# Performance work log

Hardware: AMD Instinct MI355X
Metric: run time of the kernel (lower is better)

## Reference

```python
import jax, jax.numpy as jnp
import numpy as np

B, S, DIM, HEADS, HD, FF = 2, 2048, 1024, 16, 64, 4096
PREV, MAX_SEQ, THETA, POS_BIAS_MAX, EPS = 1024, 4096, 10000.0, 2.0, 1e-6


def _freqs_cos_sin():
    inv = 1.0 / THETA ** (np.arange(0, HD, 2)[: HD // 2].astype(np.float32) / HD)
    f = np.outer(np.arange(MAX_SEQ, dtype=np.float32), inv)
    return jnp.asarray(np.cos(f), jnp.float32), jnp.asarray(np.sin(f), jnp.float32)


def setup_inputs():
    key = jax.random.key(0)
    ks = jax.random.split(key, 16)
    lin = lambda k, o, i: 0.02 * jax.random.normal(k, (o, i), jnp.float32)
    cos, sin = _freqs_cos_sin()
    return {
        "x": jax.random.normal(ks[0], (B, S, DIM), jnp.float32),
        "cache_k": jax.random.normal(ks[1], (B, HEADS, PREV, HD), jnp.float32),
        "cache_v": jax.random.normal(ks[2], (B, HEADS, PREV, HD), jnp.float32),
        "cos": cos, "sin": sin,
        "attn_norm_w": jnp.ones((DIM,), jnp.float32),
        "ffn_norm_w": jnp.ones((DIM,), jnp.float32),
        "wq": lin(ks[3], DIM, DIM), "bq": jnp.zeros((DIM,), jnp.float32),
        "wk": lin(ks[4], DIM, DIM), "bk": jnp.zeros((DIM,), jnp.float32),
        "wv": lin(ks[5], DIM, DIM), "bv": jnp.zeros((DIM,), jnp.float32),
        "wo": lin(ks[6], DIM, DIM), "bo": jnp.zeros((DIM,), jnp.float32),
        "w_gate": lin(ks[7], FF, DIM), "b_gate": jnp.zeros((FF,), jnp.float32),
        "w_value": lin(ks[8], FF, DIM), "b_value": jnp.zeros((FF,), jnp.float32),
        "w_proj": lin(ks[9], DIM, FF), "b_proj": jnp.zeros((DIM,), jnp.float32),
        "cache_limit": 3072,
    }


def _rmsnorm(h, w):
    return h * jax.lax.rsqrt(jnp.mean(h * h, axis=-1, keepdims=True) + EPS) * w


def _rope(t, cos, sin):
    # t: [B,H,L,HD]; cos/sin: [L, HD//2]; rotate interleaved pairs (complex mult)
    t2 = t.reshape(t.shape[:-1] + (HD // 2, 2))
    x0, x1 = t2[..., 0], t2[..., 1]
    c = cos[None, None]
    s = sin[None, None]
    out = jnp.stack([x0 * c - x1 * s, x0 * s + x1 * c], axis=-1)
    return out.reshape(t.shape)


def _forward(x, cache_k, cache_v, cos, sin, attn_norm_w, ffn_norm_w, wq, bq, wk, bk, wv, bv, wo, bo, w_gate, b_gate, w_value, b_value, w_proj, b_proj, cache_limit):
    b, s, d = x.shape
    h = _rmsnorm(x, attn_norm_w)
    shape4 = lambda t: t.reshape(b, s, HEADS, HD).transpose(0, 2, 1, 3)  # [B,H,S,HD]
    q = shape4(h @ wq.T + bq)
    k_new = shape4(h @ wk.T + bk)
    v_new = shape4(h @ wv.T + bv)
    k_all = jnp.concatenate([cache_k, k_new], axis=2)
    v_all = jnp.concatenate([cache_v, v_new], axis=2)
    if cache_limit > 0:
        k_all = k_all[:, :, -cache_limit:, :]
        v_all = v_all[:, :, -cache_limit:, :]
    total = k_all.shape[2]
    prev = total - s
    # RoPE: q at absolute positions prev..prev+s-1, keys at 0..total-1 (mod cache len)
    pos_q = (jnp.arange(s) + prev) % MAX_SEQ
    pos_k = jnp.arange(total) % MAX_SEQ
    q = _rope(q, cos[pos_q], sin[pos_q])
    k = _rope(k_all, cos[pos_k], sin[pos_k])
    # linear positional bias + causal mask over the new-token block only
    slope = POS_BIAS_MAX / max(total - 1, 1)
    j = jnp.arange(total, dtype=jnp.float32)[None, :]
    i_abs = (prev + jnp.arange(s, dtype=jnp.float32))[:, None]
    bias = slope * (j - i_abs)  # [s, total]
    causal = (jnp.arange(total)[None, :] - prev) > jnp.arange(s)[:, None]
    mask = jnp.where(causal, -jnp.inf, bias)
    scores = jnp.einsum('bhsd,bhtd->bhst', q, k) / jnp.sqrt(jnp.float32(HD)) + mask
    attn = jax.nn.softmax(scores, axis=-1)
    ctx = jnp.einsum('bhst,bhtd->bhsd', attn, v_all)
    ctx = ctx.transpose(0, 2, 1, 3).reshape(b, s, d)
    x = x + ctx @ wo.T + bo
    h2 = _rmsnorm(x, ffn_norm_w)
    gated = jax.nn.silu(h2 @ w_gate.T + b_gate) * (h2 @ w_value.T + b_value)
    return x + gated @ w_proj.T + b_proj


def reference(x, cache_k, cache_v, cos, sin, attn_norm_w, ffn_norm_w, wq, bq, wk, bk, wv, bv, wo, bo, w_gate, b_gate, w_value, b_value, w_proj, b_proj, cache_limit):
    return _forward(x, cache_k, cache_v, cos, sin, attn_norm_w, ffn_norm_w, wq, bq, wk, bk, wv, bv, wo, bo, w_gate, b_gate, w_value, b_value, w_proj, b_proj, cache_limit)
```

## Files before the change

kernel.cpp:

```cpp
#include <hip/hip_runtime.h>
#include <stdint.h>

typedef unsigned short u16;
typedef unsigned int   u32;
typedef __bf16 bf16x8 __attribute__((ext_vector_type(8)));
typedef float  f32x4  __attribute__((ext_vector_type(4)));
typedef u32    u32x4  __attribute__((ext_vector_type(4)));
typedef u32    u32x2  __attribute__((ext_vector_type(2)));

#define B_SZ  2
#define S_LEN 2048
#define NH    16
#define HD    64
#define DIM   1024
#define FF    4096
#define T_LEN 3072
#define PREV  1024
#define MROWS (B_SZ * S_LEN)
#define LOG2E 1.44269504f

#define MFMA16 __builtin_amdgcn_mfma_f32_16x16x32_bf16

__device__ __forceinline__ u16 f2bf(float f) {
  u32 u = __builtin_bit_cast(u32, f);
  u32 r = u + 0x7FFFu + ((u >> 16) & 1u);
  return (u16)(r >> 16);
}
__device__ __forceinline__ float bf2f(u16 h) {
  u32 u = ((u32)h) << 16;
  return __builtin_bit_cast(float, u);
}
__device__ __forceinline__ u32 cvtpk(float lo, float hi) {
  u32 r;
  asm("v_cvt_pk_bf16_f32 %0, %1, %2" : "=v"(r) : "v"(lo), "v"(hi));
  return r;
}

__device__ __forceinline__ void gl_lds16(const void* g, void* l) {
  __builtin_amdgcn_global_load_lds(
      (const __attribute__((address_space(1))) u32*)g,
      (__attribute__((address_space(3))) u32*)l, 16, 0, 0);
}

#define GFENCE() asm volatile("" ::: "memory")
#define BARF()                         \
  do {                                 \
    GFENCE();                          \
    __builtin_amdgcn_s_barrier();      \
    GFENCE();                          \
  } while (0)

__global__ __launch_bounds__(256) void cvt_kernel(const float* __restrict__ src,
                                                  u16* __restrict__ dst, int n4) {
  int i = blockIdx.x * 256 + threadIdx.x;
  const int stride = gridDim.x * 256;
  for (; i < n4; i += stride) {
    f32x4 v = *(const f32x4*)&src[(long)i * 4];
    u32x2 o;
    o[0] = (u32)f2bf(v[0]) | ((u32)f2bf(v[1]) << 16);
    o[1] = (u32)f2bf(v[2]) | ((u32)f2bf(v[3]) << 16);
    *(u32x2*)&dst[(long)i * 4] = o;
  }
}

__global__ __launch_bounds__(256) void cvt_sw_kernel(const float* __restrict__ src,
                                                     u16* __restrict__ dst, int nunits) {
  int i = blockIdx.x * 256 + threadIdx.x;
  const int stride = gridDim.x * 256;
  for (; i < nunits; i += stride) {
    int row = i >> 7;
    int g = i & 127;
    const float* s = &src[((long)row << 10) + g * 8];
    f32x4 a = *(const f32x4*)s;
    f32x4 b = *(const f32x4*)(s + 4);
    u32x4 o;
    o[0] = (u32)f2bf(a[0]) | ((u32)f2bf(a[1]) << 16);
    o[1] = (u32)f2bf(a[2]) | ((u32)f2bf(a[3]) << 16);
    o[2] = (u32)f2bf(b[0]) | ((u32)f2bf(b[1]) << 16);
    o[3] = (u32)f2bf(b[2]) | ((u32)f2bf(b[3]) << 16);
    const int gp = (g & ~7) | ((g & 7) ^ (row & 7));
    *(u32x4*)&dst[((long)row << 10) + gp * 8] = o;
  }
}

__global__ __launch_bounds__(256) void cvt_ilv_sw_kernel(const float* __restrict__ wg,
                                                         const float* __restrict__ wval,
                                                         u16* __restrict__ dst) {
  int i = blockIdx.x * 256 + threadIdx.x;
  const int stride = gridDim.x * 256;
  for (; i < FF * 128; i += stride) {
    int j = i >> 7;
    int g = i & 127;
    const float* sg = &wg[((long)j << 10) + g * 8];
    const float* sv = &wval[((long)j << 10) + g * 8];
    f32x4 a = *(const f32x4*)sg;
    f32x4 b = *(const f32x4*)(sg + 4);
    u32x4 og;
    og[0] = (u32)f2bf(a[0]) | ((u32)f2bf(a[1]) << 16);
    og[1] = (u32)f2bf(a[2]) | ((u32)f2bf(a[3]) << 16);
    og[2] = (u32)f2bf(b[0]) | ((u32)f2bf(b[1]) << 16);
    og[3] = (u32)f2bf(b[2]) | ((u32)f2bf(b[3]) << 16);
    f32x4 c = *(const f32x4*)sv;
    f32x4 d = *(const f32x4*)(sv + 4);
    u32x4 ov;
    ov[0] = (u32)f2bf(c[0]) | ((u32)f2bf(c[1]) << 16);
    ov[1] = (u32)f2bf(c[2]) | ((u32)f2bf(c[3]) << 16);
    ov[2] = (u32)f2bf(d[0]) | ((u32)f2bf(d[1]) << 16);
    ov[3] = (u32)f2bf(d[2]) | ((u32)f2bf(d[3]) << 16);
    const int rg = 2 * j, rv = 2 * j + 1;
    const int gpg = (g & ~7) | ((g & 7) ^ (rg & 7));
    const int gpv = (g & ~7) | ((g & 7) ^ (rv & 7));
    *(u32x4*)&dst[((long)rg << 10) + gpg * 8] = og;
    *(u32x4*)&dst[((long)rv << 10) + gpv * 8] = ov;
  }
}

__global__ __launch_bounds__(256) void bias_ilv_kernel(const float* __restrict__ bg,
                                                       const float* __restrict__ bval,
                                                       float* __restrict__ dst) {
  int i = blockIdx.x * 256 + threadIdx.x;
  if (i < FF) {
    dst[2 * i] = bg[i];
    dst[2 * i + 1] = bval[i];
  }
}

__global__ __launch_bounds__(256) void rmsnorm_kernel(const float* __restrict__ x,
                                                      const float* __restrict__ w,
                                                      u16* __restrict__ out) {
  const int row = blockIdx.x;
  const int tid = threadIdx.x;
  const long base = (long)row * DIM + tid * 4;
  f32x4 v = *(const f32x4*)&x[base];
  float ss = v[0] * v[0] + v[1] * v[1] + v[2] * v[2] + v[3] * v[3];
#pragma unroll
  for (int d = 1; d <= 32; d <<= 1) ss += __shfl_xor(ss, d, 64);
  __shared__ float red[4];
  if ((tid & 63) == 0) red[tid >> 6] = ss;
  __syncthreads();
  float tot = red[0] + red[1] + red[2] + red[3];
  const float sc = rsqrtf(tot * (1.f / (float)DIM) + 1e-6f);
  f32x4 wv4 = *(const f32x4*)&w[tid * 4];
  u32x2 o;
  o[0] = (u32)f2bf(v[0] * sc * wv4[0]) | ((u32)f2bf(v[1] * sc * wv4[1]) << 16);
  o[1] = (u32)f2bf(v[2] * sc * wv4[2]) | ((u32)f2bf(v[3] * sc * wv4[3]) << 16);
  const int u = tid >> 1, hf = tid & 1;
  const int up = (u & 0x78) | ((u & 7) ^ (row & 7));
  *(u32x2*)&out[(long)row * DIM + up * 8 + hf * 4] = o;
}

template <int EPI>
__global__ __launch_bounds__(512, 2) void gemm256(const u16* __restrict__ A,
                                                  const u16* __restrict__ Bw,
                                                  const float* __restrict__ bias,
                                                  u16* __restrict__ out_bf,
                                                  int N, int K) {
  __shared__ __align__(16) u16 Ab[2][256 * 64];
  __shared__ __align__(16) u16 Bb[2][256 * 64];
  const int tid = threadIdx.x;
  const int lane = tid & 63;
  const int wid = tid >> 6;
  const int wm = wid >> 2, wn = wid & 3;
  const int l15 = lane & 15, lhi = lane >> 4;
  const int c7 = l15 & 7;
  const long m0 = (long)blockIdx.y * 256;
  const long n0 = (long)blockIdx.x * 256;
  const int NT = K >> 6;

  const int srow = tid >> 3;
  const int sunit = (tid & 7) * 8;
  const u16* agp = A + (m0 + srow) * K + sunit;
  const u16* bgp = Bw + (n0 + srow) * K + sunit;
  const int ldst = tid * 8;

  auto stageA = [&](int kt, int b) {
    const int k0 = kt << 6;
    u16* d = &Ab[b][0];
#pragma unroll
    for (int c = 0; c < 4; ++c)
      gl_lds16(agp + (long)(c * 64) * K + k0, d + c * 4096 + ldst);
  };
  auto stageB = [&](int kt, int b) {
    const int k0 = kt << 6;
    u16* d = &Bb[b][0];
#pragma unroll
    for (int c = 0; c < 4; ++c)
      gl_lds16(bgp + (long)(c * 64) * K + k0, d + c * 4096 + ldst);
  };

#define READ_A(MH)                                                               \
  _Pragma("unroll") for (int m_ = 0; m_ < 4; ++m_) {                             \
    _Pragma("unroll") for (int ks_ = 0; ks_ < 2; ++ks_) {                        \
      Afr[MH][m_ * 2 + ks_] =                                                    \
          *(const bf16x8*)&Ac[(wm * 128 + (MH)*64 + m_ * 16 + l15) * 64 +        \
                              (((ks_ * 4 + lhi) ^ c7) * 8)];                     \
    }                                                                            \
  }
#define READ_B(NH)                                                               \
  _Pragma("unroll") for (int n_ = 0; n_ < 2; ++n_) {                             \
    _Pragma("unroll") for (int ks_ = 0; ks_ < 2; ++ks_) {                        \
      Bfr[NH][n_ * 2 + ks_] =                                                    \
          *(const bf16x8*)&Bc[(wn * 64 + (NH)*32 + n_ * 16 + l15) * 64 +         \
                              (((ks_ * 4 + lhi) ^ c7) * 8)];                     \
    }                                                                            \
  }
#define QUAD(MH, NH)                                                             \
  do {                                                                           \
    __builtin_amdgcn_s_setprio(1);                                               \
    _Pragma("unroll") for (int m_ = 0; m_ < 4; ++m_) {                           \
      _Pragma("unroll") for (int n_ = 0; n_ < 2; ++n_) {                         \
        acc[(MH)*4 + m_][(NH)*2 + n_] =                                          \
            MFMA16(Afr[MH][m_ * 2], Bfr[NH][n_ * 2],                             \
                   acc[(MH)*4 + m_][(NH)*2 + n_], 0, 0, 0);                      \
        acc[(MH)*4 + m_][(NH)*2 + n_] =                                          \
            MFMA16(Afr[MH][m_ * 2 + 1], Bfr[NH][n_ * 2 + 1],                     \
                   acc[(MH)*4 + m_][(NH)*2 + n_], 0, 0, 0);                      \
      }                                                                          \
    }                                                                            \
    __builtin_amdgcn_s_setprio(0);                                               \
  } while (0)

  f32x4 acc[8][4] = {};

  stageA(0, 0);
  stageB(0, 0);
  stageA(1, 1);
  stageB(1, 1);
  asm volatile("s_waitcnt vmcnt(8)" ::: "memory");
  __builtin_amdgcn_s_barrier();
  GFENCE();

  for (int kt = 0; kt < NT; ++kt) {
    const int b = kt & 1;
    const u16* Ac = &Ab[b][0];
    const u16* Bc = &Bb[b][0];
    bf16x8 Afr[2][8], Bfr[2][4];
    READ_A(0);
    READ_B(0);
    BARF();
    QUAD(0, 0);
    BARF();
    READ_A(1);
    READ_B(1);
    BARF();
    QUAD(0, 1);
    BARF();
    if (kt + 2 < NT) stageA(kt + 2, b);
    BARF();
    QUAD(1, 0);
    BARF();
    if (kt + 2 < NT) stageB(kt + 2, b);
    BARF();
    QUAD(1, 1);
    if (kt + 1 < NT) {
      if (kt + 2 < NT)
        asm volatile("s_waitcnt vmcnt(8)" ::: "memory");
      else
        asm volatile("s_waitcnt vmcnt(0)" ::: "memory");
      __builtin_amdgcn_s_barrier();
      GFENCE();
    }
  }
#undef READ_A
#undef READ_B
#undef QUAD

#pragma unroll
  for (int mi = 0; mi < 8; ++mi) {
    const long row0 = m0 + wm * 128 + mi * 16 + lhi * 4;
#pragma unroll
    for (int ni = 0; ni < 4; ++ni) {
      const long col = n0 + wn * 64 + ni * 16 + l15;
      const float bb = bias[col];
#pragma unroll
      for (int r = 0; r < 4; ++r) {
        float v = acc[mi][ni][r] + bb;
        if (EPI == 2) {
          float other = __shfl_xor(v, 1, 64);
          if (!(l15 & 1)) {
            float s = v / (1.f + __expf(-v)) * other;
            out_bf[(row0 + r) * (N >> 1) + (col >> 1)] = f2bf(s);
          }
        } else {
          out_bf[(row0 + r) * N + col] = f2bf(v);
        }
      }
    }
  }
}

template <int EPI, int NB>
__global__ __launch_bounds__(256) void gemm_bt(const u16* __restrict__ A,
                                               const u16* __restrict__ Bw,
                                               const float* __restrict__ bias,
                                               const float* __restrict__ resid,
                                               u16* __restrict__ out_bf,
                                               float* __restrict__ out_f,
                                               int N, int K) {
  constexpr int BHALF = NB / 64;
  constexpr int NFR = NB / 32;
  constexpr int LPT = 2 + BHALF;
  __shared__ __align__(16) u16 As[3][128 * 32];
  __shared__ __align__(16) u16 Bs[3][NB * 32];
  const int tid = threadIdx.x;
  const int lane = tid & 63;
  const int wv = tid >> 6;
  const int wr = wv >> 1, wc = wv & 1;
  const long m0 = (long)blockIdx.y * 128;
  const long n0 = (long)blockIdx.x * NB;

  const int arow = tid >> 2;
  const int acol = (tid & 3) << 3;
  const u16* ag = A + (m0 + arow) * K + acol;
  const u16* bg = Bw + (n0 + arow) * K + acol;
  const long hK = (long)64 * K;

  f32x4 acc[4][NFR] = {};
  const int l15 = lane & 15;
  const int lhi = lane >> 4;
  const int aoff0 = (wr * 64 + l15) * 32 + lhi * 8;
  const int boff0 = (wc * (NB / 2) + l15) * 32 + lhi * 8;
  const int nk = K >> 5;

  auto stage = [&](int t, int buf) {
    const int k0 = t << 5;
    gl_lds16(ag + k0, &As[buf][tid * 8]);
    gl_lds16(ag + k0 + hK, &As[buf][2048 + tid * 8]);
    gl_lds16(bg + k0, &Bs[buf][tid * 8]);
    if (BHALF == 2) gl_lds16(bg + k0 + hK, &Bs[buf][2048 + tid * 8]);
  };

  stage(0, 0);
  stage(1, 1);
  asm volatile("s_waitcnt vmcnt(%0)" ::"n"(LPT) : "memory");
  __builtin_amdgcn_s_barrier();
  GFENCE();

  for (int t = 0; t < nk; ++t) {
    const int cb = t % 3;
    if (t + 2 < nk) stage(t + 2, (t + 2) % 3);
    bf16x8 af[4], bfr[NFR];
#pragma unroll
    for (int i = 0; i < 4; ++i) af[i] = *(const bf16x8*)&As[cb][aoff0 + i * 16 * 32];
#pragma unroll
    for (int j = 0; j < NFR; ++j) bfr[j] = *(const bf16x8*)&Bs[cb][boff0 + j * 16 * 32];
    __builtin_amdgcn_s_setprio(1);
#pragma unroll
    for (int i = 0; i < 4; ++i)
#pragma unroll
      for (int j = 0; j < NFR; ++j)
        acc[i][j] = MFMA16(af[i], bfr[j], acc[i][j], 0, 0, 0);
    __builtin_amdgcn_s_setprio(0);
    if (t + 2 < nk) {
      asm volatile("s_waitcnt vmcnt(%0)" ::"n"(LPT) : "memory");
      __builtin_amdgcn_s_barrier();
      GFENCE();
    } else if (t + 1 < nk) {
      asm volatile("s_waitcnt vmcnt(0)" ::: "memory");
      __builtin_amdgcn_s_barrier();
      GFENCE();
    }
  }

#pragma unroll
  for (int i = 0; i < 4; ++i) {
    const long row0 = m0 + wr * 64 + i * 16 + lhi * 4;
#pragma unroll
    for (int j = 0; j < NFR; ++j) {
      const long col = n0 + wc * (NB / 2) + j * 16 + l15;
      const float bb = bias[col];
#pragma unroll
      for (int r = 0; r < 4; ++r) {
        const long idx = (row0 + r) * N + col;
        float v = acc[i][j][r] + bb;
        if (EPI == 0) out_bf[idx] = f2bf(v);
        else          out_f[idx] = resid[idx] + v;
      }
    }
  }
}

__global__ __launch_bounds__(256) void rope_q_kernel(const u16* __restrict__ qkv,
                                                     const float* __restrict__ cosT,
                                                     const float* __restrict__ sinT,
                                                     u16* __restrict__ Q) {
  int idx = blockIdx.x * 256 + threadIdx.x;
  int u = idx & 7;
  int s = (idx >> 3) & (S_LEN - 1);
  int bh = idx >> 14;
  int b = bh >> 4, h = bh & 15;
  int pos = PREV + s;
  const float SC = 0.125f * LOG2E;
  const u16* src = qkv + ((long)(b * S_LEN + s)) * (3 * DIM) + h * HD + u * 8;
  u32x4 d = *(const u32x4*)src;
  f32x4 cv = *(const f32x4*)&cosT[(long)pos * 32 + u * 4];
  f32x4 sv = *(const f32x4*)&sinT[(long)pos * 32 + u * 4];
  u32x4 o;
#pragma unroll
  for (int p = 0; p < 4; ++p) {
    float x0 = bf2f((u16)(d[p] & 0xffff));
    float x1 = bf2f((u16)(d[p] >> 16));
    float y0 = (x0 * cv[p] - x1 * sv[p]) * SC;
    float y1 = (x0 * sv[p] + x1 * cv[p]) * SC;
    o[p] = (u32)f2bf(y0) | ((u32)f2bf(y1) << 16);
  }
  *(u32x4*)&Q[((long)bh * S_LEN + s) * HD + u * 8] = o;
}

__global__ __launch_bounds__(256) void rope_k_kernel(const u16* __restrict__ qkv,
                                                     const float* __restrict__ cache_k,
                                                     const float* __restrict__ cosT,
                                                     const float* __restrict__ sinT,
                                                     u16* __restrict__ Kall) {
  int idx = blockIdx.x * 256 + threadIdx.x;
  int u = idx & 7;
  int t2 = idx >> 3;
  int j = t2 % T_LEN;
  int bh = t2 / T_LEN;
  int b = bh >> 4, h = bh & 15;
  float e[8];
  if (j < PREV) {
    const float* src = cache_k + ((long)bh * PREV + j) * HD + u * 8;
    f32x4 a = *(const f32x4*)src;
    f32x4 c = *(const f32x4*)(src + 4);
    e[0] = a[0]; e[1] = a[1]; e[2] = a[2]; e[3] = a[3];
    e[4] = c[0]; e[5] = c[1]; e[6] = c[2]; e[7] = c[3];
  } else {
    const u16* src = qkv + ((long)(b * S_LEN + (j - PREV))) * (3 * DIM) + DIM + h * HD + u * 8;
    u32x4 d = *(const u32x4*)src;
#pragma unroll
    for (int p = 0; p < 4; ++p) {
      e[2 * p] = bf2f((u16)(d[p] & 0xffff));
      e[2 * p + 1] = bf2f((u16)(d[p] >> 16));
    }
  }
  f32x4 cv = *(const f32x4*)&cosT[(long)j * 32 + u * 4];
  f32x4 sv = *(const f32x4*)&sinT[(long)j * 32 + u * 4];
  u32x4 o;
#pragma unroll
  for (int p = 0; p < 4; ++p) {
    float y0 = e[2 * p] * cv[p] - e[2 * p + 1] * sv[p];
    float y1 = e[2 * p] * sv[p] + e[2 * p + 1] * cv[p];
    o[p] = (u32)f2bf(y0) | ((u32)f2bf(y1) << 16);
  }
  *(u32x4*)&Kall[((long)bh * T_LEN + j) * HD + (u ^ (j & 7)) * 8] = o;
}

__global__ __launch_bounds__(256) void build_vt_kernel(const u16* __restrict__ qkv,
                                                       const float* __restrict__ cache_v,
                                                       u16* __restrict__ Vtg) {
  int idx = blockIdx.x * 256 + threadIdx.x;
  int hd = idx & 63;
  int t2 = idx >> 6;
  int kb = t2 % 384;
  int bh = t2 / 384;
  int b = bh >> 4, h = bh & 15;
  int key0 = kb * 8;
  u16 vals[8];
  if (key0 < PREV) {
#pragma unroll
    for (int i = 0; i < 8; ++i)
      vals[i] = f2bf(cache_v[((long)bh * PREV + key0 + i) * HD + hd]);
  } else {
#pragma unroll
    for (int i = 0; i < 8; ++i)
      vals[i] = qkv[((long)(b * S_LEN + key0 + i - PREV)) * (3 * DIM) + 2 * DIM + h * HD + hd];
  }
  u32x4 o;
#pragma unroll
  for (int p = 0; p < 4; ++p)
    o[p] = (u32)vals[2 * p] | ((u32)vals[2 * p + 1] << 16);
  const int span = kb >> 3;
  const int u = (kb & 7) ^ (hd & 7);
  *(u32x4*)&Vtg[((long)bh * HD + hd) * T_LEN + span * 64 + u * 8] = o;
}

__global__ __launch_bounds__(256, 4) void attn_kernel(const u16* __restrict__ Q,
                                                      const u16* __restrict__ Kg,
                                                      const u16* __restrict__ Vtg,
                                                      u16* __restrict__ ctx, float slope2) {
  __shared__ __align__(16) u16 Ks[2][64 * 64];
  __shared__ __align__(16) u16 Vs[2][64 * 64];
  __shared__ __align__(16) u16 Ps[4][16 * 64];

  const int tid = threadIdx.x;
  const int lane = tid & 63;
  const int wv = tid >> 6;
  const int l15 = lane & 15;
  const int lhi = lane >> 4;
  const int c7 = l15 & 7;
  const int bh = blockIdx.x;
  const int qt = blockIdx.y;
  const int b = bh >> 4, h = bh & 15;
  const int q0 = qt * 64;
  const int nt = (PREV + q0 + 64) >> 6;

  const long qrow = (long)bh * S_LEN + q0 + wv * 16 + l15;
  bf16x8 aq0 = *(const bf16x8*)&Q[qrow * HD + lhi * 8];
  bf16x8 aq1 = *(const bf16x8*)&Q[qrow * HD + 32 + lhi * 8];

  const long kgb = (long)bh * T_LEN * HD;
  const long vgb = (long)bh * HD * T_LEN;
  const int srow = tid >> 3;
  const int sunit = (tid & 7) * 8;

  gl_lds16(&Kg[kgb + (long)srow * HD + sunit], &Ks[0][tid * 8]);
  gl_lds16(&Kg[kgb + (long)(srow + 32) * HD + sunit], &Ks[0][2048 + tid * 8]);
  gl_lds16(&Vtg[vgb + (long)srow * T_LEN + sunit], &Vs[0][tid * 8]);
  gl_lds16(&Vtg[vgb + (long)(srow + 32) * T_LEN + sunit], &Vs[0][2048 + tid * 8]);
  __syncthreads();

  f32x4 o[4] = {};
  float mrun = -1e30f, lrun = 0.f;
  const int iabs = PREV + q0 + wv * 16 + l15;
  u16* Pw = &Ps[wv][0];

  for (int t = 0; t < nt; ++t) {
    const int cur = t & 1, nxt = cur ^ 1;
    const int kt0 = t << 6;
    if (t + 1 < nt) {
      const int kn = kt0 + 64;
      gl_lds16(&Kg[kgb + (long)(kn + srow) * HD + sunit], &Ks[nxt][tid * 8]);
      gl_lds16(&Kg[kgb + (long)(kn + srow + 32) * HD + sunit], &Ks[nxt][2048 + tid * 8]);
      gl_lds16(&Vtg[vgb + (long)srow * T_LEN + kn + sunit], &Vs[nxt][tid * 8]);
      gl_lds16(&Vtg[vgb + (long)(srow + 32) * T_LEN + kn + sunit], &Vs[nxt][2048 + tid * 8]);
    }

    f32x4 sf[4];
    __builtin_amdgcn_s_setprio(1);
#pragma unroll
    for (int jf = 0; jf < 4; ++jf) {
      const int krow = jf * 16 + l15;
      bf16x8 ak0 = *(const bf16x8*)&Ks[cur][krow * 64 + ((lhi ^ c7) * 8)];
      bf16x8 ak1 = *(const bf16x8*)&Ks[cur][krow * 64 + (((4 + lhi) ^ c7) * 8)];
      f32x4 s = {};
      s = MFMA16(ak0, aq0, s, 0, 0, 0);
      s = MFMA16(ak1, aq1, s, 0, 0, 0);
      sf[jf] = s;
    }
    __builtin_amdgcn_s_setprio(0);

    const bool masked = (t == nt - 1);
#pragma unroll
    for (int jf = 0; jf < 4; ++jf)
#pragma unroll
      for (int r = 0; r < 4; ++r) {
        const int jcol = kt0 + jf * 16 + 4 * lhi + r;
        float s_ = sf[jf][r] + slope2 * (float)(jcol - iabs);
        sf[jf][r] = (masked && jcol > iabs) ? -1e30f : s_;
      }

    float t0 = fmaxf(fmaxf(sf[0][0], sf[0][1]), fmaxf(sf[0][2], sf[0][3]));
    float t1 = fmaxf(fmaxf(sf[1][0], sf[1][1]), fmaxf(sf[1][2], sf[1][3]));
    float t2 = fmaxf(fmaxf(sf[2][0], sf[2][1]), fmaxf(sf[2][2], sf[2][3]));
    float t3 = fmaxf(fmaxf(sf[3][0], sf[3][1]), fmaxf(sf[3][2], sf[3][3]));
    float pmax = fmaxf(fmaxf(t0, t1), fmaxf(t2, t3));
    pmax = fmaxf(pmax, __shfl_xor(pmax, 16, 64));
    pmax = fmaxf(pmax, __shfl_xor(pmax, 32, 64));

    if (!__all(pmax - mrun <= 8.f)) {
      float mnew = fmaxf(mrun, pmax);
      float scl = exp2f(mrun - mnew);
      mrun = mnew;
      lrun *= scl;
#pragma unroll
      for (int r = 0; r < 4; ++r) {
        float sr = __shfl(scl, 4 * lhi + r, 64);
#pragma unroll
        for (int hf = 0; hf < 4; ++hf) o[hf][r] *= sr;
      }
    }

    float ps = 0.f;
#pragma unroll
    for (int jf = 0; jf < 4; ++jf) {
      f32x4 p;
#pragma unroll
      for (int r = 0; r < 4; ++r) {
        p[r] = exp2f(sf[jf][r] - mrun);
        ps += p[r];
      }
      u32x2 pw2;
      pw2[0] = cvtpk(p[0], p[1]);
      pw2[1] = cvtpk(p[2], p[3]);
      const int u = (2 * jf + (lhi >> 1)) ^ c7;
      *(u32x2*)&Pw[l15 * 64 + u * 8 + (lhi & 1) * 4] = pw2;
    }
    ps += __shfl_xor(ps, 16, 64);
    ps += __shfl_xor(ps, 32, 64);
    lrun += ps;

    bf16x8 pa0 = *(const bf16x8*)&Pw[l15 * 64 + ((lhi ^ c7) * 8)];
    bf16x8 pa1 = *(const bf16x8*)&Pw[l15 * 64 + (((4 + lhi) ^ c7) * 8)];
    __builtin_amdgcn_s_setprio(1);
#pragma unroll
    for (int hf = 0; hf < 4; ++hf) {
      const int vrow = hf * 16 + l15;
      bf16x8 bv0 = *(const bf16x8*)&Vs[cur][vrow * 64 + ((lhi ^ c7) * 8)];
      bf16x8 bv1 = *(const bf16x8*)&Vs[cur][vrow * 64 + (((4 + lhi) ^ c7) * 8)];
      o[hf] = MFMA16(pa0, bv0, o[hf], 0, 0, 0);
      o[hf] = MFMA16(pa1, bv1, o[hf], 0, 0, 0);
    }
    __builtin_amdgcn_s_setprio(0);
    __syncthreads();
  }

#pragma unroll
  for (int r = 0; r < 4; ++r) {
    const float inv = 1.f / __shfl(lrun, 4 * lhi + r, 64);
    const long srow_ = (long)b * S_LEN + q0 + wv * 16 + 4 * lhi + r;
#pragma unroll
    for (int hf = 0; hf < 4; ++hf)
      ctx[srow_ * DIM + h * HD + hf * 16 + l15] = f2bf(o[hf][r] * inv);
  }
}

extern "C" void kernel_launch(void* const* d_in, const int* in_sizes, int n_in,
                              void* d_out, int out_size, void* d_ws, size_t ws_size,
                              hipStream_t stream) {
  (void)in_sizes; (void)n_in; (void)out_size; (void)ws_size;
  const float* x       = (const float*)d_in[0];
  const float* cache_k = (const float*)d_in[1];
  const float* cache_v = (const float*)d_in[2];
  const float* cosT    = (const float*)d_in[3];
  const float* sinT    = (const float*)d_in[4];
  const float* attn_w  = (const float*)d_in[5];
  const float* ffn_w   = (const float*)d_in[6];
  const float* wq      = (const float*)d_in[7];
  const float* bq      = (const float*)d_in[8];
  const float* wk      = (const float*)d_in[9];
  const float* bk      = (const float*)d_in[10];
  const float* wv_     = (const float*)d_in[11];
  const float* bv      = (const float*)d_in[12];
  const float* wo      = (const float*)d_in[13];
  const float* bo      = (const float*)d_in[14];
  const float* wg      = (const float*)d_in[15];
  const float* bg      = (const float*)d_in[16];
  const float* wval    = (const float*)d_in[17];
  const float* bval    = (const float*)d_in[18];
  const float* wp      = (const float*)d_in[19];
  const float* bp      = (const float*)d_in[20];
  float* out = (float*)d_out;

  char* w = (char*)d_ws;
  size_t off = 0;
  auto alloc = [&](size_t bytes) -> char* {
    char* p = w + off;
    off += (bytes + 255) & ~(size_t)255;
    return p;
  };
  u16*   wqkv_bf  = (u16*)alloc((size_t)3 * DIM * DIM * 2);
  u16*   wo_bf    = (u16*)alloc((size_t)DIM * DIM * 2);
  u16*   wgv_bf   = (u16*)alloc((size_t)2 * FF * DIM * 2);
  u16*   wproj_bf = (u16*)alloc((size_t)DIM * FF * 2);
  float* bqkv     = (float*)alloc((size_t)3 * DIM * 4);
  float* bgv      = (float*)alloc((size_t)2 * FF * 4);
  float* x2       = (float*)alloc((size_t)MROWS * DIM * 4);
  char* AR = alloc((size_t)117440512);
  u16* qkv   = (u16*)(AR + 0);
  u16* Qb    = (u16*)(AR + 25165824);
  u16* Kb    = (u16*)(AR + 33554432);
  u16* Vtg   = (u16*)(AR + 46137344);
  u16* h1    = (u16*)(AR + 58720256);
  u16* ctx   = (u16*)(AR + 0);
  u16* h2    = (u16*)(AR + 8388608);
  u16* gated = (u16*)(AR + 16777216);

  cvt_sw_kernel<<<512, 256, 0, stream>>>(wq, wqkv_bf, DIM * DIM / 8);
  cvt_sw_kernel<<<512, 256, 0, stream>>>(wk, wqkv_bf + DIM * DIM, DIM * DIM / 8);
  cvt_sw_kernel<<<512, 256, 0, stream>>>(wv_, wqkv_bf + 2 * DIM * DIM, DIM * DIM / 8);
  cvt_kernel<<<512, 256, 0, stream>>>(wo, wo_bf, DIM * DIM / 4);
  cvt_ilv_sw_kernel<<<1024, 256, 0, stream>>>(wg, wval, wgv_bf);
  cvt_kernel<<<1024, 256, 0, stream>>>(wp, wproj_bf, DIM * FF / 4);
  bias_ilv_kernel<<<16, 256, 0, stream>>>(bg, bval, bgv);
  hipMemcpyAsync(bqkv, bq, DIM * 4, hipMemcpyDeviceToDevice, stream);
  hipMemcpyAsync(bqkv + DIM, bk, DIM * 4, hipMemcpyDeviceToDevice, stream);
  hipMemcpyAsync(bqkv + 2 * DIM, bv, DIM * 4, hipMemcpyDeviceToDevice, stream);

  rmsnorm_kernel<<<MROWS, 256, 0, stream>>>(x, attn_w, h1);
  gemm256<0><<<dim3(12, 16), 512, 0, stream>>>(h1, wqkv_bf, bqkv, qkv, 3 * DIM, DIM);
  rope_q_kernel<<<2048, 256, 0, stream>>>(qkv, cosT, sinT, Qb);
  rope_k_kernel<<<3072, 256, 0, stream>>>(qkv, cache_k, cosT, sinT, Kb);
  build_vt_kernel<<<3072, 256, 0, stream>>>(qkv, cache_v, Vtg);
  attn_kernel<<<dim3(B_SZ * NH, S_LEN / 64), 256, 0, stream>>>(
      Qb, Kb, Vtg, ctx, (2.0f / (float)(T_LEN - 1)) * LOG2E);
  gemm_bt<1, 64><<<dim3(16, 32), 256, 0, stream>>>(ctx, wo_bf, bo, x, nullptr, x2,
                                                   DIM, DIM);
  rmsnorm_kernel<<<MROWS, 256, 0, stream>>>(x2, ffn_w, h2);
  gemm256<2><<<dim3(32, 16), 512, 0, stream>>>(h2, wgv_bf, bgv, gated, 2 * FF, DIM);
  gemm_bt<1, 64><<<dim3(16, 32), 256, 0, stream>>>(gated, wproj_bf, bp, x2, nullptr, out,
                                                   DIM, FF);
}
```

Baseline: 386.9 us.

## Hoist positional bias out of attention loop and compute row sums via MFMA

Splits the linear positional bias into a per-tile constant offset (tracked through a running scalar folded into the max) and a precomputed per-lane column term, so the per-element bias arithmetic and the full bias add before the max reduction are removed. The causal mask is applied only on the last tile. Softmax row sums are computed with an extra MFMA against a ones vector instead of shuffle reductions. Pointer increments replace per-iteration address math, and the trailing barrier is skipped on the last iteration. The max now uses an upper bound (raw score max plus maximum bias), so the rescale threshold is looser and sums come from bf16-rounded probabilities, which slightly changes numerics.

```diff
diff --git a/kernel.cpp b/kernel.cpp
--- a/kernel.cpp
+++ b/kernel.cpp
@@ -504,26 +504,48 @@
   const int srow = tid >> 3;
   const int sunit = (tid & 7) * 8;
 
-  gl_lds16(&Kg[kgb + (long)srow * HD + sunit], &Ks[0][tid * 8]);
-  gl_lds16(&Kg[kgb + (long)(srow + 32) * HD + sunit], &Ks[0][2048 + tid * 8]);
-  gl_lds16(&Vtg[vgb + (long)srow * T_LEN + sunit], &Vs[0][tid * 8]);
-  gl_lds16(&Vtg[vgb + (long)(srow + 32) * T_LEN + sunit], &Vs[0][2048 + tid * 8]);
+  const u16* kst = Kg + kgb + (long)srow * HD + sunit;
+  const u16* vst = Vtg + vgb + (long)srow * T_LEN + sunit;
+
+  gl_lds16(kst, &Ks[0][tid * 8]);
+  gl_lds16(kst + 32 * HD, &Ks[0][2048 + tid * 8]);
+  gl_lds16(vst, &Vs[0][tid * 8]);
+  gl_lds16(vst + (long)32 * T_LEN, &Vs[0][2048 + tid * 8]);
+  kst += 64 * HD;
+  vst += 64;
   __syncthreads();
 
   f32x4 o[4] = {};
-  float mrun = -1e30f, lrun = 0.f;
-  const int iabs = PREV + q0 + wv * 16 + l15;
+  f32x4 lrun = {0.f, 0.f, 0.f, 0.f};
+  float mrun = -1e30f;
+  const int qq = wv * 16 + l15;
   u16* Pw = &Ps[wv][0];
+
+  f32x4 be[4];
+#pragma unroll
+  for (int jf = 0; jf < 4; ++jf)
+#pragma unroll
+    for (int r = 0; r < 4; ++r)
+      be[jf][r] = slope2 * (float)(jf * 16 + 4 * lhi + r);
+  const float bmax = slope2 * 63.f;
+
+  bf16x8 vones;
+#pragma unroll
+  for (int e = 0; e < 8; ++e) vones[e] = (__bf16)1.0f;
+
+  float ktf = 0.f;
+  const float kstep = slope2 * 64.f;
 
   for (int t = 0; t < nt; ++t) {
     const int cur = t & 1, nxt = cur ^ 1;
-    const int kt0 = t << 6;
-    if (t + 1 < nt) {
-      const int kn = kt0 + 64;
-      gl_lds16(&Kg[kgb + (long)(kn + srow) * HD + sunit], &Ks[nxt][tid * 8]);
-      gl_lds16(&Kg[kgb + (long)(kn + srow + 32) * HD + sunit], &Ks[nxt][2048 + tid * 8]);
-      gl_lds16(&Vtg[vgb + (long)srow * T_LEN + kn + sunit], &Vs[nxt][tid * 8]);
-      gl_lds16(&Vtg[vgb + (long)(srow + 32) * T_LEN + kn + sunit], &Vs[nxt][2048 + tid * 8]);
+    const bool last = (t == nt - 1);
+    if (!last) {
+      gl_lds16(kst, &Ks[nxt][tid * 8]);
+      gl_lds16(kst + 32 * HD, &Ks[nxt][2048 + tid * 8]);
+      gl_lds16(vst, &Vs[nxt][tid * 8]);
+      gl_lds16(vst + (long)32 * T_LEN, &Vs[nxt][2048 + tid * 8]);
+      kst += 64 * HD;
+      vst += 64;
     }
 
     f32x4 sf[4];
@@ -540,59 +562,56 @@
     }
     __builtin_amdgcn_s_setprio(0);
 
-    const bool masked = (t == nt - 1);
-#pragma unroll
-    for (int jf = 0; jf < 4; ++jf)
+    if (last) {
+#pragma unroll
+      for (int jf = 0; jf < 4; ++jf)
+#pragma unroll
+        for (int r = 0; r < 4; ++r)
+          if (jf * 16 + 4 * lhi + r > qq) sf[jf][r] = -1e30f;
+    }
+
+    float h0 = fmaxf(fmaxf(sf[0][0], sf[0][1]), fmaxf(sf[0][2], sf[0][3]));
+    float h1 = fmaxf(fmaxf(sf[1][0], sf[1][1]), fmaxf(sf[1][2], sf[1][3]));
+    float h2 = fmaxf(fmaxf(sf[2][0], sf[2][1]), fmaxf(sf[2][2], sf[2][3]));
+    float h3 = fmaxf(fmaxf(sf[3][0], sf[3][1]), fmaxf(sf[3][2], sf[3][3]));
+    float pm = fmaxf(fmaxf(h0, h1), fmaxf(h2, h3));
+    pm = fmaxf(pm, __shfl_xor(pm, 16, 64));
+    pm = fmaxf(pm, __shfl_xor(pm, 32, 64));
+    const float pmax_abs = pm + ktf + bmax;
+
+    if (!__all(pmax_abs - mrun <= 8.f)) {
+      const float mnew = fmaxf(mrun, pmax_abs);
+      const float scl = exp2f(mrun - mnew);
+      mrun = mnew;
 #pragma unroll
       for (int r = 0; r < 4; ++r) {
-        const int jcol = kt0 + jf * 16 + 4 * lhi + r;
-        float s_ = sf[jf][r] + slope2 * (float)(jcol - iabs);
-        sf[jf][r] = (masked && jcol > iabs) ? -1e30f : s_;
-      }
-
-    float t0 = fmaxf(fmaxf(sf[0][0], sf[0][1]), fmaxf(sf[0][2], sf[0][3]));
-    float t1 = fmaxf(fmaxf(sf[1][0], sf[1][1]), fmaxf(sf[1][2], sf[1][3]));
-    float t2 = fmaxf(fmaxf(sf[2][0], sf[2][1]), fmaxf(sf[2][2], sf[2][3]));
-    float t3 = fmaxf(fmaxf(sf[3][0], sf[3][1]), fmaxf(sf[3][2], sf[3][3]));
-    float pmax = fmaxf(fmaxf(t0, t1), fmaxf(t2, t3));
-    pmax = fmaxf(pmax, __shfl_xor(pmax, 16, 64));
-    pmax = fmaxf(pmax, __shfl_xor(pmax, 32, 64));
-
-    if (!__all(pmax - mrun <= 8.f)) {
-      float mnew = fmaxf(mrun, pmax);
-      float scl = exp2f(mrun - mnew);
-      mrun = mnew;
-      lrun *= scl;
-#pragma unroll
-      for (int r = 0; r < 4; ++r) {
-        float sr = __shfl(scl, 4 * lhi + r, 64);
+        const float sr = __shfl(scl, 4 * lhi + r, 64);
+        lrun[r] *= sr;
 #pragma unroll
         for (int hf = 0; hf < 4; ++hf) o[hf][r] *= sr;
       }
     }
-
-    float ps = 0.f;
+    const float meff = mrun - ktf;
+
 #pragma unroll
     for (int jf = 0; jf < 4; ++jf) {
       f32x4 p;
 #pragma unroll
-      for (int r = 0; r < 4; ++r) {
-        p[r] = exp2f(sf[jf][r] - mrun);
-        ps += p[r];
-      }
+      for (int r = 0; r < 4; ++r)
+        p[r] = exp2f(sf[jf][r] + (be[jf][r] - meff));
       u32x2 pw2;
       pw2[0] = cvtpk(p[0], p[1]);
       pw2[1] = cvtpk(p[2], p[3]);
       const int u = (2 * jf + (lhi >> 1)) ^ c7;
       *(u32x2*)&Pw[l15 * 64 + u * 8 + (lhi & 1) * 4] = pw2;
     }
-    ps += __shfl_xor(ps, 16, 64);
-    ps += __shfl_xor(ps, 32, 64);
-    lrun += ps;
 
     bf16x8 pa0 = *(const bf16x8*)&Pw[l15 * 64 + ((lhi ^ c7) * 8)];
     bf16x8 pa1 = *(const bf16x8*)&Pw[l15 * 64 + (((4 + lhi) ^ c7) * 8)];
+    f32x4 psum = {};
     __builtin_amdgcn_s_setprio(1);
+    psum = MFMA16(pa0, vones, psum, 0, 0, 0);
+    psum = MFMA16(pa1, vones, psum, 0, 0, 0);
 #pragma unroll
     for (int hf = 0; hf < 4; ++hf) {
       const int vrow = hf * 16 + l15;
@@ -602,12 +621,15 @@
       o[hf] = MFMA16(pa1, bv1, o[hf], 0, 0, 0);
     }
     __builtin_amdgcn_s_setprio(0);
-    __syncthreads();
+    lrun += psum;
+
+    ktf += kstep;
+    if (!last) __syncthreads();
   }
 
 #pragma unroll
   for (int r = 0; r < 4; ++r) {
-    const float inv = 1.f / __shfl(lrun, 4 * lhi + r, 64);
+    const float inv = 1.f / lrun[r];
     const long srow_ = (long)b * S_LEN + q0 + wv * 16 + 4 * lhi + r;
 #pragma unroll
     for (int hf = 0; hf < 4; ++hf)
```

Result: no change. 383.2 us (-1.0%).
